# Kernel optimization log

Hardware: AMD Instinct MI355X
Metric: run time of the kernel (lower is better)

The kernel has to match this reference:

```python
import jax, jax.numpy as jnp
import numpy as np

N_NODES = 50000
N_EDGES = 800000
D_IN = 128
D_OUT = 128


def setup_inputs() -> dict:
    key = jax.random.key(0)
    k1, k2, k3, k4, k5 = jax.random.split(key, 5)
    x = jax.random.normal(k1, (N_NODES, D_IN), dtype=jnp.float32)
    weight = jax.random.normal(k2, (D_IN, D_OUT), dtype=jnp.float32)
    bias = jax.random.normal(k3, (D_OUT,), dtype=jnp.float32)
    vals = jax.random.uniform(k4, (N_EDGES,), dtype=jnp.float32)
    row = jax.random.randint(k5, (N_EDGES,), 0, N_NODES, dtype=jnp.int32)
    col = jax.random.randint(jax.random.fold_in(k5, 1), (N_EDGES,), 0, N_NODES, dtype=jnp.int32)
    return {"x": x, "weight": weight, "bias": bias, "vals": vals, "row": row, "col": col}


def reference(x, weight, bias, vals, row, col):
    # Dense feature transform: x @ W   [N, D_out]
    h = x @ weight
    # SpMM: out[i] = sum_{e: row[e]==i} vals[e] * h[col[e]]
    msg = vals[:, None] * h[col]  # [E, D_out]
    out = jax.ops.segment_sum(msg, row, num_segments=N_NODES)
    # Fused bias + ReLU (original: out += bias; relu(out))
    out = jax.nn.relu(out + bias)
    return out
```

## Files before the change

### kernel.cpp

```cpp
#include <hip/hip_runtime.h>

#define N_NODES 50000
#define N_EDGES 800000
#define D 128
#define D4 32

#define BIN_LOG 5
#define BIN_ROWS 32
#define NBINS ((N_NODES + BIN_ROWS - 1) / BIN_ROWS)
#define CAP 704

#define NKEYS 256

#define EPB 4096
#define NCHUNK ((N_EDGES + EPB - 1) / EPB)
#define GEMM_BLOCKS ((N_NODES + 63) / 64)
#define E4 (N_EDGES / 4)
#define CNTROW 1568

typedef __attribute__((ext_vector_type(8))) short bf16x8;
typedef __attribute__((ext_vector_type(4))) float f32x4;

__device__ __forceinline__ unsigned bf16_1(float a) {
    unsigned u = __float_as_uint(a);
    return (u + 0x7fffu + ((u >> 16) & 1u)) >> 16;
}
__device__ __forceinline__ unsigned pack_bf16(float a, float b) {
    return bf16_1(a) | (bf16_1(b) << 16);
}
__device__ __forceinline__ float ubf_lo(unsigned u) {
    return __uint_as_float(u << 16);
}
__device__ __forceinline__ float ubf_hi(unsigned u) {
    return __uint_as_float(u & 0xffff0000u);
}

__global__ __launch_bounds__(256) void count_and_prep(
        const int4* __restrict__ rowi4, const float* __restrict__ w,
        unsigned* __restrict__ wtu, ushort* __restrict__ cnt_t) {
    if (blockIdx.x >= NCHUNK) {
        const int i = (blockIdx.x - NCHUNK) * 256 + threadIdx.x;
        if (i < D * 64) {
            const int col = i >> 6;
            const int k2  = i & 63;
            wtu[i] = pack_bf16(w[(size_t)(2 * k2) * D + col],
                               w[(size_t)(2 * k2 + 1) * D + col]);
        }
        return;
    }

    __shared__ int hist[NBINS];
    const int tid = threadIdx.x;
    for (int i = tid; i < NBINS; i += 256) hist[i] = 0;
    __syncthreads();

    #pragma unroll
    for (int q = 0; q < 4; ++q) {
        const int i4 = blockIdx.x * (EPB / 4) + q * 256 + tid;
        if (i4 < E4) {
            const int4 r = rowi4[i4];
            atomicAdd(&hist[r.x >> BIN_LOG], 1);
            atomicAdd(&hist[r.y >> BIN_LOG], 1);
            atomicAdd(&hist[r.z >> BIN_LOG], 1);
            atomicAdd(&hist[r.w >> BIN_LOG], 1);
        }
    }
    __syncthreads();

    ushort* ct = cnt_t + (size_t)blockIdx.x * CNTROW;
    for (int i = tid; i < NBINS; i += 256) ct[i] = (ushort)hist[i];
}

__global__ __launch_bounds__(256) void scan_chunks(const ushort* __restrict__ cnt_t,
                                                   ushort* __restrict__ base_t,
                                                   int* __restrict__ total) {
    __shared__ int wsum[4], woff[4];
    const int bin = blockIdx.x;
    const int tid = threadIdx.x;

    int v = 0;
    if (tid < NCHUNK) v = cnt_t[(size_t)tid * CNTROW + bin];
    int incl = v;
    #pragma unroll
    for (int off = 1; off < 64; off <<= 1) {
        const int t = __shfl_up(incl, off);
        if ((tid & 63) >= off) incl += t;
    }
    if ((tid & 63) == 63) wsum[tid >> 6] = incl;
    __syncthreads();
    if (tid == 0) {
        int run = 0;
        #pragma unroll
        for (int w2 = 0; w2 < 4; ++w2) { woff[w2] = run; run += wsum[w2]; }
    }
    __syncthreads();
    incl += woff[tid >> 6];
    if (tid < NCHUNK) base_t[(size_t)tid * CNTROW + bin] = (ushort)(incl - v);
    if (tid == 255) total[bin] = incl;
}

__global__ __launch_bounds__(256) void place_and_gemm(
        const float4* __restrict__ x4, const uint4* __restrict__ wt4,
        ushort* __restrict__ hb,
        const int4* __restrict__ rowi4, const int4* __restrict__ coli4,
        const float4* __restrict__ vals4,
        const ushort* __restrict__ base_t, uint2* __restrict__ bins) {

    if (blockIdx.x < NCHUNK) {
        __shared__ int sbase[NBINS];
        __shared__ int cur[NBINS];
        const int tid = threadIdx.x;
        const ushort* br = base_t + (size_t)blockIdx.x * CNTROW;
        for (int i = tid; i < NBINS; i += 256) { sbase[i] = br[i]; cur[i] = 0; }
        __syncthreads();

        union { int4 v4[4]; int a[16]; } R, C;
        union { float4 v4[4]; float a[16]; } V;
        const int base4 = blockIdx.x * (EPB / 4);
        #pragma unroll
        for (int q = 0; q < 4; ++q) {
            const int i4  = base4 + q * 256 + tid;
            const int i4c = (i4 < E4) ? i4 : (E4 - 1);
            R.v4[q] = rowi4[i4c];
            C.v4[q] = coli4[i4c];
            V.v4[q] = vals4[i4c];
            if (i4 >= E4) R.v4[q] = make_int4(-1, -1, -1, -1);
        }

        #pragma unroll
        for (int q = 0; q < 16; ++q) {
            const int r = R.a[q];
            if (r >= 0) {
                const int b   = r >> BIN_LOG;
                const int pos = sbase[b] + atomicAdd(&cur[b], 1);
                const unsigned c = (unsigned)C.a[q];
                if (pos < CAP)
                    bins[(size_t)b * CAP + pos] =
                        make_uint2((c << 16) | bf16_1(V.a[q]),
                                   ((unsigned)(r & (BIN_ROWS - 1)) << 3) | (c >> 13));
            }
        }
        return;
    }

    const int bid  = blockIdx.x - NCHUNK;
    const int lane = threadIdx.x & 63;
    const int r0   = bid * 64 + (threadIdx.x >> 6) * 16;
    const int arow = r0 + (lane & 15);
    const int kg   = lane >> 4;
    const bool rok = (arow < N_NODES);

    bf16x8 afr[4];
    #pragma unroll
    for (int kc = 0; kc < 4; ++kc) {
        float4 f0 = make_float4(0.f, 0.f, 0.f, 0.f);
        float4 f1 = f0;
        if (rok) {
            const int c4 = kc * 8 + kg * 2;
            f0 = x4[(size_t)arow * D4 + c4];
            f1 = x4[(size_t)arow * D4 + c4 + 1];
        }
        union { bf16x8 v; unsigned u[4]; } a;
        a.u[0] = pack_bf16(f0.x, f0.y);
        a.u[1] = pack_bf16(f0.z, f0.w);
        a.u[2] = pack_bf16(f1.x, f1.y);
        a.u[3] = pack_bf16(f1.z, f1.w);
        afr[kc] = a.v;
    }

    f32x4 acc[8];
    #pragma unroll
    for (int t = 0; t < 8; ++t) acc[t] = (f32x4){0.f, 0.f, 0.f, 0.f};

    #pragma unroll
    for (int t = 0; t < 8; ++t) {
        const int col = t * 16 + (lane & 15);
        #pragma unroll
        for (int kc = 0; kc < 4; ++kc) {
            union { bf16x8 v; uint4 u; } b;
            b.u = wt4[(size_t)col * 16 + kc * 4 + kg];
            acc[t] = __builtin_amdgcn_mfma_f32_16x16x32_bf16(afr[kc], b.v,
                                                             acc[t], 0, 0, 0);
        }
    }

    #pragma unroll
    for (int t = 0; t < 8; ++t) {
        const int col = t * 16 + (lane & 15);
        #pragma unroll
        for (int j = 0; j < 4; ++j) {
            const int r = r0 + (lane >> 4) * 4 + j;
            if (r < N_NODES)
                hb[(size_t)r * D + col] = (ushort)bf16_1(acc[t][j]);
        }
    }
}

__global__ __launch_bounds__(256) void sort_gather(const int* __restrict__ total,
                                                   const uint2* __restrict__ bins,
                                                   const uint2* __restrict__ hb2,
                                                   const float4* __restrict__ bias4,
                                                   float4* __restrict__ out4) {
    __shared__ int      hcnt[NKEYS];
    __shared__ int      cur[NKEYS];
    __shared__ int      starts[NKEYS + 1];
    __shared__ int      wsum[4], woff[4];
    __shared__ unsigned sorted[CAP];

    const int bin = blockIdx.x;
    const int tid = threadIdx.x;
    int n = total[bin];
    n = (n > CAP) ? CAP : n;
    const unsigned long long* brec8 =
        (const unsigned long long*)(bins + (size_t)bin * CAP);

    hcnt[tid] = 0;
    cur[tid] = 0;
    __syncthreads();

    const bool v0 = (tid       < n);
    const bool v1 = (tid + 256 < n);
    const bool v2 = (tid + 512 < n);
    unsigned long long r0 = 0, r1 = 0, r2 = 0;
    if (v0) r0 = __builtin_nontemporal_load(brec8 + tid);
    if (v1) r1 = __builtin_nontemporal_load(brec8 + tid + 256);
    if (v2) r2 = __builtin_nontemporal_load(brec8 + tid + 512);

    if (v0) atomicAdd(&hcnt[(unsigned)(r0 >> 32) & (NKEYS - 1)], 1);
    if (v1) atomicAdd(&hcnt[(unsigned)(r1 >> 32) & (NKEYS - 1)], 1);
    if (v2) atomicAdd(&hcnt[(unsigned)(r2 >> 32) & (NKEYS - 1)], 1);
    __syncthreads();

    {
        int v = hcnt[tid];
        #pragma unroll
        for (int off = 1; off < 64; off <<= 1) {
            const int t = __shfl_up(v, off);
            if ((tid & 63) >= off) v += t;
        }
        starts[tid + 1] = v;
        if ((tid & 63) == 63) wsum[tid >> 6] = v;
    }
    __syncthreads();
    if (tid == 0) {
        int run = 0;
        #pragma unroll
        for (int w2 = 0; w2 < 4; ++w2) { woff[w2] = run; run += wsum[w2]; }
        starts[0] = 0;
    }
    __syncthreads();
    starts[tid + 1] += woff[tid >> 6];
    __syncthreads();

    if (v0) {
        const int key = (unsigned)(r0 >> 32) & (NKEYS - 1);
        const int dst = starts[key] + atomicAdd(&cur[key], 1);
        if (dst < CAP) sorted[dst] = (unsigned)r0;
    }
    if (v1) {
        const int key = (unsigned)(r1 >> 32) & (NKEYS - 1);
        const int dst = starts[key] + atomicAdd(&cur[key], 1);
        if (dst < CAP) sorted[dst] = (unsigned)r1;
    }
    if (v2) {
        const int key = (unsigned)(r2 >> 32) & (NKEYS - 1);
        const int dst = starts[key] + atomicAdd(&cur[key], 1);
        if (dst < CAP) sorted[dst] = (unsigned)r2;
    }
    __syncthreads();

    const int wave = tid >> 6;
    const int lane = tid & 63;
    const int half = lane >> 5;
    const int hl   = lane & 31;
    const float4 b = bias4[hl];

    #pragma unroll
    for (int rp = 0; rp < 4; ++rp) {
        const int row  = rp * 8 + half * 4 + wave;
        const int node = bin * BIN_ROWS + row;
        int s = 0, len = 0;
        if (node < N_NODES) {
            s   = starts[row << 3];
            len = starts[(row << 3) + 8] - s;
        }
        int lm = len;
        lm = max(lm, __shfl_xor(lm, 32));

        float4 acc = {0.f, 0.f, 0.f, 0.f};
        for (int j0 = 0; j0 < lm; j0 += 8) {
            uint2 hv[8];
            float vv[8];
            #pragma unroll
            for (int q = 0; q < 8; ++q) {
                const int jq = j0 + q;
                const int jj = (jq < len) ? (s + jq) : 0;
                unsigned ed = sorted[jj];
                ed = (jq < len) ? ed : 0u;
                vv[q] = __uint_as_float((ed & 0xffffu) << 16);
                hv[q] = hb2[(size_t)(ed >> 16) * 32 + hl];
            }
            #pragma unroll
            for (int q = 0; q < 8; ++q) {
                acc.x = fmaf(vv[q], ubf_lo(hv[q].x), acc.x);
                acc.y = fmaf(vv[q], ubf_hi(hv[q].x), acc.y);
                acc.z = fmaf(vv[q], ubf_lo(hv[q].y), acc.z);
                acc.w = fmaf(vv[q], ubf_hi(hv[q].y), acc.w);
            }
        }
        if (node < N_NODES) {
            f32x4 o;
            o[0] = fmaxf(acc.x + b.x, 0.f);
            o[1] = fmaxf(acc.y + b.y, 0.f);
            o[2] = fmaxf(acc.z + b.z, 0.f);
            o[3] = fmaxf(acc.w + b.w, 0.f);
            __builtin_nontemporal_store(o, (f32x4*)(out4 + (size_t)node * 32 + hl));
        }
    }
}

extern "C" void kernel_launch(void* const* d_in, const int* in_sizes, int n_in,
                              void* d_out, int out_size, void* d_ws, size_t ws_size,
                              hipStream_t stream) {
    const float* x      = (const float*)d_in[0];
    const float* weight = (const float*)d_in[1];
    const float* bias   = (const float*)d_in[2];
    const float* vals   = (const float*)d_in[3];
    const int*   rowi   = (const int*)d_in[4];
    const int*   coli   = (const int*)d_in[5];
    float* out = (float*)d_out;

    char* w = (char*)d_ws;
    ushort*   hb     = (ushort*)w;   w += (size_t)N_NODES * D * sizeof(ushort);
    unsigned* wt     = (unsigned*)w; w += (size_t)D * 64 * sizeof(unsigned);
    ushort*   cnt_t  = (ushort*)w;   w += (size_t)NCHUNK * CNTROW * sizeof(ushort);
    ushort*   base_t = (ushort*)w;   w += (size_t)NCHUNK * CNTROW * sizeof(ushort);
    int*      total  = (int*)w;      w += ((size_t)NBINS + 16) * sizeof(int);
    uint2*    bins   = (uint2*)w;

    count_and_prep<<<NCHUNK + 32, 256, 0, stream>>>((const int4*)rowi, weight,
                                                    wt, cnt_t);

    scan_chunks<<<NBINS, 256, 0, stream>>>(cnt_t, base_t, total);

    place_and_gemm<<<NCHUNK + GEMM_BLOCKS, 256, 0, stream>>>(
        (const float4*)x, (const uint4*)wt, hb,
        (const int4*)rowi, (const int4*)coli, (const float4*)vals,
        base_t, bins);

    sort_gather<<<NBINS, 256, 0, stream>>>(total, bins, (const uint2*)hb,
                                           (const float4*)bias, (float4*)out);
}
```

Measured before the change: 70.98 us.

## Split bf16 feature table into column quarters and gather per quarter

The bf16 h matrix is now stored as four column-quarter planes of 32 features each, and the gather kernel runs four blocks per bin, each handling one quarter. Each quarter plane is 3.2 MB, so the intent is that the working set of random row gathers stays in cache. Within a wave, 8 lanes cover the quarter's features and 4 lane groups handle different edges, and the partial sums are reduced with shuffles. The cost is that each bin's local sort is repeated four times, plus extra shuffle work and smaller 64-byte gather segments.

```diff
diff --git a/kernel.cpp b/kernel.cpp
--- a/kernel.cpp
+++ b/kernel.cpp
@@ -101,7 +101,7 @@
 
 __global__ __launch_bounds__(256) void place_and_gemm(
         const float4* __restrict__ x4, const uint4* __restrict__ wt4,
-        ushort* __restrict__ hb,
+        ushort* __restrict__ hbq,
         const int4* __restrict__ rowi4, const int4* __restrict__ coli4,
         const float4* __restrict__ vals4,
         const ushort* __restrict__ base_t, uint2* __restrict__ bins) {
@@ -187,18 +187,20 @@
     #pragma unroll
     for (int t = 0; t < 8; ++t) {
         const int col = t * 16 + (lane & 15);
+        const int qq  = col >> 5;
+        const int cq  = col & 31;
         #pragma unroll
         for (int j = 0; j < 4; ++j) {
             const int r = r0 + (lane >> 4) * 4 + j;
             if (r < N_NODES)
-                hb[(size_t)r * D + col] = (ushort)bf16_1(acc[t][j]);
+                hbq[((size_t)qq * N_NODES + r) * 32 + cq] = (ushort)bf16_1(acc[t][j]);
         }
     }
 }
 
 __global__ __launch_bounds__(256) void sort_gather(const int* __restrict__ total,
                                                    const uint2* __restrict__ bins,
-                                                   const uint2* __restrict__ hb2,
+                                                   const ushort* __restrict__ hbq,
                                                    const float4* __restrict__ bias4,
                                                    float4* __restrict__ out4) {
     __shared__ int      hcnt[NKEYS];
@@ -207,7 +209,8 @@
     __shared__ int      wsum[4], woff[4];
     __shared__ unsigned sorted[CAP];
 
-    const int bin = blockIdx.x;
+    const int bin = blockIdx.x >> 2;
+    const int qq  = blockIdx.x & 3;
     const int tid = threadIdx.x;
     int n = total[bin];
     n = (n > CAP) ? CAP : n;
@@ -269,11 +272,13 @@
     }
     __syncthreads();
 
+    const uint2* hq2 = (const uint2*)(hbq + (size_t)qq * N_NODES * 32);
     const int wave = tid >> 6;
     const int lane = tid & 63;
     const int half = lane >> 5;
-    const int hl   = lane & 31;
-    const float4 b = bias4[hl];
+    const int eg   = (lane & 31) >> 3;
+    const int fl   = lane & 7;
+    const float4 b = bias4[qq * 8 + fl];
 
     #pragma unroll
     for (int rp = 0; rp < 4; ++rp) {
@@ -289,32 +294,35 @@
 
         float4 acc = {0.f, 0.f, 0.f, 0.f};
         for (int j0 = 0; j0 < lm; j0 += 8) {
-            uint2 hv[8];
-            float vv[8];
             #pragma unroll
-            for (int q = 0; q < 8; ++q) {
-                const int jq = j0 + q;
-                const int jj = (jq < len) ? (s + jq) : 0;
+            for (int u = 0; u < 2; ++u) {
+                const int j  = j0 + u * 4 + eg;
+                const int jj = (j < len) ? (s + j) : 0;
                 unsigned ed = sorted[jj];
-                ed = (jq < len) ? ed : 0u;
-                vv[q] = __uint_as_float((ed & 0xffffu) << 16);
-                hv[q] = hb2[(size_t)(ed >> 16) * 32 + hl];
+                ed = (j < len) ? ed : 0u;
+                const float v = __uint_as_float((ed & 0xffffu) << 16);
+                const uint2 hv = hq2[(size_t)(ed >> 16) * 8 + fl];
+                acc.x = fmaf(v, ubf_lo(hv.x), acc.x);
+                acc.y = fmaf(v, ubf_hi(hv.x), acc.y);
+                acc.z = fmaf(v, ubf_lo(hv.y), acc.z);
+                acc.w = fmaf(v, ubf_hi(hv.y), acc.w);
             }
-            #pragma unroll
-            for (int q = 0; q < 8; ++q) {
-                acc.x = fmaf(vv[q], ubf_lo(hv[q].x), acc.x);
-                acc.y = fmaf(vv[q], ubf_hi(hv[q].x), acc.y);
-                acc.z = fmaf(vv[q], ubf_lo(hv[q].y), acc.z);
-                acc.w = fmaf(vv[q], ubf_hi(hv[q].y), acc.w);
-            }
-        }
-        if (node < N_NODES) {
+        }
+        #pragma unroll
+        for (int off = 8; off <= 16; off <<= 1) {
+            acc.x += __shfl_xor(acc.x, off);
+            acc.y += __shfl_xor(acc.y, off);
+            acc.z += __shfl_xor(acc.z, off);
+            acc.w += __shfl_xor(acc.w, off);
+        }
+        if (node < N_NODES && eg == 0) {
             f32x4 o;
             o[0] = fmaxf(acc.x + b.x, 0.f);
             o[1] = fmaxf(acc.y + b.y, 0.f);
             o[2] = fmaxf(acc.z + b.z, 0.f);
             o[3] = fmaxf(acc.w + b.w, 0.f);
-            __builtin_nontemporal_store(o, (f32x4*)(out4 + (size_t)node * 32 + hl));
+            __builtin_nontemporal_store(o,
+                (f32x4*)(out4 + (size_t)node * 32 + qq * 8 + fl));
         }
     }
 }
@@ -331,7 +339,7 @@
     float* out = (float*)d_out;
 
     char* w = (char*)d_ws;
-    ushort*   hb     = (ushort*)w;   w += (size_t)N_NODES * D * sizeof(ushort);
+    ushort*   hbq    = (ushort*)w;   w += (size_t)N_NODES * D * sizeof(ushort);
     unsigned* wt     = (unsigned*)w; w += (size_t)D * 64 * sizeof(unsigned);
     ushort*   cnt_t  = (ushort*)w;   w += (size_t)NCHUNK * CNTROW * sizeof(ushort);
     ushort*   base_t = (ushort*)w;   w += (size_t)NCHUNK * CNTROW * sizeof(ushort);
@@ -344,10 +352,10 @@
     scan_chunks<<<NBINS, 256, 0, stream>>>(cnt_t, base_t, total);
 
     place_and_gemm<<<NCHUNK + GEMM_BLOCKS, 256, 0, stream>>>(
-        (const float4*)x, (const uint4*)wt, hb,
+        (const float4*)x, (const uint4*)wt, hbq,
         (const int4*)rowi, (const int4*)coli, (const float4*)vals,
         base_t, bins);
 
-    sort_gather<<<NBINS, 256, 0, stream>>>(total, bins, (const uint2*)hb,
-                                           (const float4*)bias, (float4*)out);
-}
+    sort_gather<<<NBINS * 4, 256, 0, stream>>>(total, bins, hbq,
+                                               (const float4*)bias, (float4*)out);
+}
```

New measurement: 75.02 us. 1.06x slower.
